# Kernel tuning notes

Measured on AMD Instinct MI355X. Metric: run time of the kernel, lower is better.

## Reference

```python
import jax, jax.numpy as jnp
import numpy as np

H = 1024


def _gru_dir(xg, h0, w_hh, b_hh, reverse):
    # xg: (L, G, 3H) precomputed input-gate projections; h0: (G, H)
    def step(h, xt):
        hg = h @ w_hh.T + b_hh
        xr, xz, xn = jnp.split(xt, 3, axis=-1)
        hr, hz, hn = jnp.split(hg, 3, axis=-1)
        r = jax.nn.sigmoid(xr + hr)
        z = jax.nn.sigmoid(xz + hz)
        n = jnp.tanh(xn + r * hn)
        h_new = (1.0 - z) * n + z * h
        return h_new, h_new
    _, hs = jax.lax.scan(step, h0, xg, reverse=reverse)
    return hs  # (L, G, H), time-ordered (scan reverse keeps original order)


def setup_inputs() -> dict:
    key = jax.random.key(0)
    ks = jax.random.split(key, 12)
    N, G, L = 16384, 256, 128
    s = 1.0 / np.sqrt(H)
    inp = {
        "h_atom": jax.random.normal(ks[0], (N, H), dtype=jnp.float32),
        "batch": jnp.sort(jax.random.randint(ks[1], (N,), 0, G)),
        "bias": jax.random.uniform(ks[2], (H,), jnp.float32, -s, s),
        "w_ih_f": jax.random.uniform(ks[3], (3 * H, H), jnp.float32, -s, s),
        "w_hh_f": jax.random.uniform(ks[4], (3 * H, H), jnp.float32, -s, s),
        "b_ih_f": jax.random.uniform(ks[5], (3 * H,), jnp.float32, -s, s),
        "b_hh_f": jax.random.uniform(ks[6], (3 * H,), jnp.float32, -s, s),
        "w_ih_b": jax.random.uniform(ks[7], (3 * H, H), jnp.float32, -s, s),
        "w_hh_b": jax.random.uniform(ks[8], (3 * H, H), jnp.float32, -s, s),
        "b_ih_b": jax.random.uniform(ks[9], (3 * H,), jnp.float32, -s, s),
        "b_hh_b": jax.random.uniform(ks[10], (3 * H,), jnp.float32, -s, s),
        "num_graphs": G,
        "pad_len": L,
    }
    return inp


def reference(h_atom, bias, w_ih_f, w_hh_f, b_ih_f, b_hh_f,
              w_ih_b, w_hh_b, b_ih_b, b_hh_b, batch, num_graphs, pad_len):
    N = h_atom.shape[0]
    G, L = num_graphs, pad_len
    message = jax.nn.relu(h_atom + bias)  # (N, H)

    # per-graph counts / positions (batch is sorted by graph id)
    counts = jax.ops.segment_sum(jnp.ones((N,), jnp.int32), batch, num_segments=G)
    start = jnp.cumsum(counts) - counts
    pos = jnp.arange(N) - start[batch]  # position of each atom within its graph

    # pad ragged atoms -> (G, L, H); padded slots stay zero (matches torch)
    msgs = jnp.zeros((G, L, H), h_atom.dtype).at[batch, pos].set(message)

    # segment-max hidden init, shared by both directions
    h0 = jax.ops.segment_max(h_atom, batch, num_segments=G)  # (G, H)
    h0 = jnp.where(counts[:, None] > 0, h0, 0.0)

    # precompute input-gate projections, time-major
    xg_f = jnp.einsum('glh,kh->lgk', msgs, w_ih_f) + b_ih_f  # (L, G, 3H)
    xg_b = jnp.einsum('glh,kh->lgk', msgs, w_ih_b) + b_ih_b

    hs_f = _gru_dir(xg_f, h0, w_hh_f, b_hh_f, reverse=False)  # (L, G, H)
    hs_b = _gru_dir(xg_b, h0, w_hh_b, b_hh_b, reverse=True)   # (L, G, H)

    h_messages = jnp.concatenate([hs_f, hs_b], axis=-1).transpose(1, 0, 2)  # (G, L, 2H)

    # unpad back to (N, 2H)
    return h_messages[batch, pos]
```

## Files before the change

### kernel.cpp

```cpp
#include <hip/hip_runtime.h>
#include <stdint.h>

#define H 1024
#define G_ 256
#define LPAD 128

typedef float  floatx4 __attribute__((ext_vector_type(4)));
typedef short  shortx8 __attribute__((ext_vector_type(8)));

#define MFMA(a, b, c) __builtin_amdgcn_mfma_f32_16x16x32_bf16((a), (b), (c), 0, 0, 0)

__device__ __forceinline__ uint16_t f2bf(float f) {
  union { float f; uint32_t i; } v; v.f = f;
  uint32_t r = (v.i + 0x7FFFu + ((v.i >> 16) & 1u)) >> 16;
  return (uint16_t)r;
}
__device__ __forceinline__ float bf2f(uint16_t u) {
  union { uint32_t i; float f; } v; v.i = ((uint32_t)u) << 16; return v.f;
}
__device__ __forceinline__ float sigmoid_(float x) { return 1.f / (1.f + __expf(-x)); }
__device__ __forceinline__ float tanh_(float x) {
  float ax = fabsf(x);
  float e = __expf(2.f * ax);
  float t = 1.f - 2.f / (e + 1.f);
  return x >= 0.f ? t : -t;
}

__global__ void k_f2b(const float* __restrict__ src, uint16_t* __restrict__ dst) {
  size_t i = ((size_t)blockIdx.x * blockDim.x + threadIdx.x) * 8;
  float4 a = *(const float4*)(src + i);
  float4 b = *(const float4*)(src + i + 4);
  uint16_t o[8] = {f2bf(a.x), f2bf(a.y), f2bf(a.z), f2bf(a.w),
                   f2bf(b.x), f2bf(b.y), f2bf(b.z), f2bf(b.w)};
  uint4 ov; __builtin_memcpy(&ov, o, 16);
  *(uint4*)(dst + i) = ov;
}

__global__ void k_setup(const int* __restrict__ batch, int N, int* __restrict__ start,
                        int* __restrict__ bar) {
  int g = threadIdx.x;
  if (g < 512) bar[g] = 0;
  if (g > G_) return;
  int lo = 0, hi = N;
  while (lo < hi) { int mid = (lo + hi) >> 1; if (batch[mid] < g) lo = mid + 1; else hi = mid; }
  start[g] = lo;
}

__global__ void k_msg(const float* __restrict__ h_atom, const float* __restrict__ bias,
                      uint16_t* __restrict__ msg) {
  int row = blockIdx.x, t = threadIdx.x;
  size_t off = (size_t)row * H + t * 8;
  float4 h0 = *(const float4*)(h_atom + off);
  float4 h1 = *(const float4*)(h_atom + off + 4);
  float4 b0 = *(const float4*)(bias + t * 8);
  float4 b1 = *(const float4*)(bias + t * 8 + 4);
  float v[8] = {h0.x + b0.x, h0.y + b0.y, h0.z + b0.z, h0.w + b0.w,
                h1.x + b1.x, h1.y + b1.y, h1.z + b1.z, h1.w + b1.w};
  uint16_t o[8];
#pragma unroll
  for (int i = 0; i < 8; i++) o[i] = f2bf(v[i] > 0.f ? v[i] : 0.f);
  uint4 ov; __builtin_memcpy(&ov, o, 16);
  *(uint4*)(msg + off) = ov;
}

__global__ void k_h0(const float* __restrict__ h_atom, const int* __restrict__ start,
                     float* __restrict__ hf32, uint16_t* __restrict__ hbf) {
  int g = blockIdx.x, t = threadIdx.x;
  int s = start[g], e = start[g + 1];
  float m[4] = {-INFINITY, -INFINITY, -INFINITY, -INFINITY};
  const float* base = h_atom + t * 4;
  for (int a = s; a < e; a++) {
    float4 v = *(const float4*)(base + (size_t)a * H);
    m[0] = fmaxf(m[0], v.x); m[1] = fmaxf(m[1], v.y);
    m[2] = fmaxf(m[2], v.z); m[3] = fmaxf(m[3], v.w);
  }
  if (s == e) { m[0] = m[1] = m[2] = m[3] = 0.f; }
#pragma unroll
  for (int i = 0; i < 4; i++) {
    int c = t * 4 + i;
    float mv = m[i];
    uint16_t bv = f2bf(mv);
    hf32[(size_t)0 * G_ * H + (size_t)g * H + c] = mv;
    hf32[(size_t)2 * G_ * H + (size_t)g * H + c] = mv;
    hbf [(size_t)0 * G_ * H + (size_t)g * H + c] = bv;
    hbf [(size_t)2 * G_ * H + (size_t)g * H + c] = bv;
  }
}

__global__ __launch_bounds__(256) void k_gemm_xg(
    const uint16_t* __restrict__ A, const uint16_t* __restrict__ Wf,
    const uint16_t* __restrict__ Wb, uint16_t* __restrict__ C, int N) {
  __shared__ __align__(16) uint16_t SM[128 * 128];
  uint16_t* As = SM;
  uint16_t* Bs = SM + 128 * 64;
  int bn = blockIdx.x, bm = blockIdx.y;
  const uint16_t* B = (bn < 24) ? Wf : Wb;
  int brow = (bn < 24 ? bn : bn - 24) * 128;
  int tid = threadIdx.x, wid = tid >> 6, lane = tid & 63;
  int wm = wid >> 1, wn = wid & 1;
  floatx4 acc[4][4];
#pragma unroll
  for (int mi = 0; mi < 4; mi++)
#pragma unroll
    for (int ni = 0; ni < 4; ni++) acc[mi][ni] = (floatx4){0.f, 0.f, 0.f, 0.f};
  int arow = bm * 128;
  for (int kb = 0; kb < H; kb += 64) {
    uint4 av[4], bv[4];
#pragma unroll
    for (int p = 0; p < 4; p++) {
      int c = p * 256 + tid;
      av[p] = *(const uint4*)(A + (size_t)(arow + (c >> 3)) * H + kb + (c & 7) * 8);
      bv[p] = *(const uint4*)(B + (size_t)(brow + (c >> 3)) * H + kb + (c & 7) * 8);
    }
    __syncthreads();
#pragma unroll
    for (int p = 0; p < 4; p++) {
      int c = p * 256 + tid;
      *(uint4*)(As + (size_t)c * 8) = av[p];
      *(uint4*)(Bs + (size_t)c * 8) = bv[p];
    }
    __syncthreads();
#pragma unroll
    for (int ks = 0; ks < 2; ks++) {
      const uint16_t* ab = As + ((wm * 64 + (lane & 15)) * 64 + ks * 32 + (lane >> 4) * 8);
      const uint16_t* bb = Bs + ((wn * 64 + (lane & 15)) * 64 + ks * 32 + (lane >> 4) * 8);
      shortx8 af[4], bfr[4];
#pragma unroll
      for (int i = 0; i < 4; i++) {
        af[i]  = *(const shortx8*)(ab + i * 16 * 64);
        bfr[i] = *(const shortx8*)(bb + i * 16 * 64);
      }
#pragma unroll
      for (int mi = 0; mi < 4; mi++)
#pragma unroll
        for (int ni = 0; ni < 4; ni++)
          acc[mi][ni] = MFMA(af[mi], bfr[ni], acc[mi][ni]);
    }
  }
  __syncthreads();
  int crow = wm * 64 + (lane >> 4) * 4;
  int ccol = wn * 64 + (lane & 15);
#pragma unroll
  for (int mi = 0; mi < 4; mi++)
#pragma unroll
    for (int ni = 0; ni < 4; ni++)
#pragma unroll
      for (int r = 0; r < 4; r++)
        SM[(crow + mi * 16 + r) * 128 + ccol + ni * 16] = f2bf(acc[mi][ni][r]);
  __syncthreads();
#pragma unroll
  for (int p = 0; p < 8; p++) {
    int c = p * 256 + tid;
    int row = c >> 4, col = (c & 15) * 8;
    *(uint4*)(C + (size_t)(arow + row) * 6144 + bn * 128 + col) =
        *(const uint4*)(SM + row * 128 + col);
  }
}

__global__ __launch_bounds__(256) void k_gru(
    const uint16_t* __restrict__ xg,
    const uint16_t* __restrict__ whf, const uint16_t* __restrict__ whb,
    const float* __restrict__ bihf, const float* __restrict__ bhhf,
    const float* __restrict__ bihb, const float* __restrict__ bhhb,
    float* __restrict__ hf32, uint16_t* __restrict__ hbf,
    const int* __restrict__ start, float* __restrict__ out,
    int* bar) {
  __shared__ __align__(16) uint16_t As[64 * 64];
  __shared__ __align__(16) uint16_t Bs[96 * 64];
  __shared__ float HG[64 * 97];
  int b = blockIdx.x;
  int e = b & 7, hi = b >> 3;
  int d = e >> 2, jm = e & 3;
  int jc = (hi & 7) * 4 + jm;
  int g0 = (hi >> 3) * 64;
  int grp = d * 4 + (hi >> 3);
  const uint16_t* W = d ? whb : whf;
  int tid = threadIdx.x, wid = tid >> 6, lane = tid & 63;
  int wm = wid >> 1, wn = wid & 1;

  int base = tid * 8;
  int gl = base >> 5, j0 = base & 31;
  int g = g0 + gl;
  int s = start[g], cnt = start[g + 1] - s;
  int col0 = jc * 32 + j0;
  const float* bih = d ? bihb : bihf;
  const float* bhh = d ? bhhb : bhhf;
  float br8[8], bz8[8], bni8[8], bnh8[8];
#pragma unroll
  for (int i = 0; i < 8; i++) {
    int c = col0 + i;
    br8[i] = bih[c] + bhh[c];
    bz8[i] = bih[H + c] + bhh[H + c];
    bni8[i] = bih[2 * H + c];
    bnh8[i] = bhh[2 * H + c];
  }

  int a_row[2], aw_off[2];
#pragma unroll
  for (int p = 0; p < 2; p++) {
    int c = p * 256 + tid, row = c >> 3;
    a_row[p] = row;
    aw_off[p] = row * 128 + (((tid & 7) * 16) ^ ((row & 7) << 4));
  }
  int b_wrow[3], bw_off[3];
#pragma unroll
  for (int p = 0; p < 3; p++) {
    int c = p * 256 + tid, row = c >> 3;
    b_wrow[p] = (row >> 5) * H + jc * 32 + (row & 31);
    bw_off[p] = row * 128 + (((tid & 7) * 16) ^ ((row & 7) << 4));
  }
  int xm = (lane & 7) << 4;
  int arow0 = (wm * 32 + (lane & 15)) * 128;
  int brow0 = (wn * 48 + (lane & 15)) * 128;
  int kchunk = (tid & 7) * 8;

  for (int l = 0; l < LPAD; l++) {
    int cur = l & 1;
    const uint16_t* hsrc = hbf + (size_t)(d * 2 + cur) * G_ * H;
    int t = d ? (LPAD - 1 - l) : l;
    bool active = (t < cnt);

    uint4 xr8 = {0, 0, 0, 0}, xz8 = {0, 0, 0, 0}, xn8 = {0, 0, 0, 0};
    if (active) {
      const uint16_t* xp = xg + (size_t)(s + t) * 6144 + (size_t)d * 3072 + col0;
      xr8 = *(const uint4*)xp;
      xz8 = *(const uint4*)(xp + H);
      xn8 = *(const uint4*)(xp + 2 * H);
    }
    const float* h_old = hf32 + ((size_t)(d * 2 + cur) * G_ + g) * H + col0;
    float4 ho0 = *(const float4*)h_old;
    float4 ho1 = *(const float4*)(h_old + 4);

    floatx4 acc[2][3];
#pragma unroll
    for (int mi = 0; mi < 2; mi++)
#pragma unroll
      for (int ni = 0; ni < 3; ni++) acc[mi][ni] = (floatx4){0.f, 0.f, 0.f, 0.f};

    uint4 av[2], bv[3];
#pragma unroll
    for (int p = 0; p < 2; p++)
      av[p] = *(const uint4*)(hsrc + (size_t)(g0 + a_row[p]) * H + kchunk);
#pragma unroll
    for (int p = 0; p < 3; p++)
      bv[p] = *(const uint4*)(W + (size_t)b_wrow[p] * H + kchunk);

    for (int kb = 0; kb < 16; kb++) {
      __syncthreads();
#pragma unroll
      for (int p = 0; p < 2; p++) *(uint4*)((char*)As + aw_off[p]) = av[p];
#pragma unroll
      for (int p = 0; p < 3; p++) *(uint4*)((char*)Bs + bw_off[p]) = bv[p];
      __syncthreads();
      if (kb < 15) {
        int ko = (kb + 1) * 64 + kchunk;
#pragma unroll
        for (int p = 0; p < 2; p++)
          av[p] = *(const uint4*)(hsrc + (size_t)(g0 + a_row[p]) * H + ko);
#pragma unroll
        for (int p = 0; p < 3; p++)
          bv[p] = *(const uint4*)(W + (size_t)b_wrow[p] * H + ko);
      }
#pragma unroll
      for (int ks = 0; ks < 2; ks++) {
        int o = (ks * 64 + (lane >> 4) * 16) ^ xm;
        shortx8 a0 = *(const shortx8*)((const char*)As + arow0 + o);
        shortx8 a1 = *(const shortx8*)((const char*)As + arow0 + 2048 + o);
#pragma unroll
        for (int ni = 0; ni < 3; ni++) {
          shortx8 bf_ = *(const shortx8*)((const char*)Bs + brow0 + ni * 2048 + o);
          acc[0][ni] = MFMA(a0, bf_, acc[0][ni]);
          acc[1][ni] = MFMA(a1, bf_, acc[1][ni]);
        }
      }
    }
    __syncthreads();
#pragma unroll
    for (int mi = 0; mi < 2; mi++)
#pragma unroll
      for (int ni = 0; ni < 3; ni++) {
        int row0 = wm * 32 + mi * 16 + (lane >> 4) * 4;
        int col = wn * 48 + ni * 16 + (lane & 15);
#pragma unroll
        for (int r = 0; r < 4; r++) HG[(row0 + r) * 97 + col] = acc[mi][ni][r];
      }
    __syncthreads();

    float hv[8] = {ho0.x, ho0.y, ho0.z, ho0.w, ho1.x, ho1.y, ho1.z, ho1.w};
    const uint16_t* xru = (const uint16_t*)&xr8;
    const uint16_t* xzu = (const uint16_t*)&xz8;
    const uint16_t* xnu = (const uint16_t*)&xn8;
    float o32[8]; uint16_t ob[8];
#pragma unroll
    for (int i = 0; i < 8; i++) {
      float hr = HG[gl * 97 + j0 + i];
      float hz = HG[gl * 97 + 32 + j0 + i];
      float hn = HG[gl * 97 + 64 + j0 + i];
      float r = sigmoid_(bf2f(xru[i]) + hr + br8[i]);
      float z = sigmoid_(bf2f(xzu[i]) + hz + bz8[i]);
      float n = tanh_(bf2f(xnu[i]) + bni8[i] + r * (hn + bnh8[i]));
      float hnew = (1.f - z) * n + z * hv[i];
      o32[i] = hnew;
      ob[i] = f2bf(hnew);
    }
    float* h_new32 = hf32 + ((size_t)(d * 2 + (cur ^ 1)) * G_ + g) * H + col0;
    uint16_t* h_newb = hbf + ((size_t)(d * 2 + (cur ^ 1)) * G_ + g) * H + col0;
    *(float4*)h_new32 = make_float4(o32[0], o32[1], o32[2], o32[3]);
    *(float4*)(h_new32 + 4) = make_float4(o32[4], o32[5], o32[6], o32[7]);
    uint4 obv; __builtin_memcpy(&obv, ob, 16);
    *(uint4*)h_newb = obv;
    if (active) {
      float* op = out + (size_t)(s + t) * 2048 + (size_t)d * H + col0;
      *(float4*)op = make_float4(o32[0], o32[1], o32[2], o32[3]);
      *(float4*)(op + 4) = make_float4(o32[4], o32[5], o32[6], o32[7]);
    }

    if (l + 1 < LPAD) {
      __syncthreads();
      if (tid == 0) {
        __threadfence();
        __hip_atomic_fetch_add(&bar[grp * 32], 1, __ATOMIC_RELEASE, __HIP_MEMORY_SCOPE_AGENT);
        int tgt = (l + 1) * 32;
        while (__hip_atomic_load(&bar[grp * 32], __ATOMIC_RELAXED, __HIP_MEMORY_SCOPE_AGENT) < tgt)
          __builtin_amdgcn_s_sleep(2);
        __threadfence();
      }
      __syncthreads();
    }
  }
}

extern "C" void kernel_launch(void* const* d_in, const int* in_sizes, int n_in,
                              void* d_out, int out_size, void* d_ws, size_t ws_size,
                              hipStream_t stream) {
  const float* h_atom = (const float*)d_in[0];
  const int*   batch  = (const int*)d_in[1];
  const float* bias   = (const float*)d_in[2];
  const float* w_ih_f = (const float*)d_in[3];
  const float* w_hh_f = (const float*)d_in[4];
  const float* b_ih_f = (const float*)d_in[5];
  const float* b_hh_f = (const float*)d_in[6];
  const float* w_ih_b = (const float*)d_in[7];
  const float* w_hh_b = (const float*)d_in[8];
  const float* b_ih_b = (const float*)d_in[9];
  const float* b_hh_b = (const float*)d_in[10];
  int N = in_sizes[0] / H;
  float* out = (float*)d_out;

  const size_t W3 = (size_t)3 * H * H;
  char* ws = (char*)d_ws;
  uint16_t* msg  = (uint16_t*)ws;
  uint16_t* xg   = (uint16_t*)(ws + (size_t)N * H * 2);
  char* p = ws + (size_t)N * H * 2 + (size_t)N * 6144 * 2;
  uint16_t* wihf = (uint16_t*)p; p += W3 * 2;
  uint16_t* wihb = (uint16_t*)p; p += W3 * 2;
  uint16_t* whhf = (uint16_t*)p; p += W3 * 2;
  uint16_t* whhb = (uint16_t*)p; p += W3 * 2;
  float*    hf32 = (float*)p;    p += (size_t)4 * G_ * H * 4;
  uint16_t* hbf  = (uint16_t*)p; p += (size_t)4 * G_ * H * 2;
  int*      start = (int*)p;
  int*      bar   = (int*)(p + 2048);

  int wgrid = (int)(W3 / (256 * 8));
  k_f2b<<<wgrid, 256, 0, stream>>>(w_ih_f, wihf);
  k_f2b<<<wgrid, 256, 0, stream>>>(w_ih_b, wihb);
  k_f2b<<<wgrid, 256, 0, stream>>>(w_hh_f, whhf);
  k_f2b<<<wgrid, 256, 0, stream>>>(w_hh_b, whhb);
  k_setup<<<1, 512, 0, stream>>>(batch, N, start, bar);
  k_msg<<<N, 128, 0, stream>>>(h_atom, bias, msg);
  k_h0<<<G_, 256, 0, stream>>>(h_atom, start, hf32, hbf);
  k_gemm_xg<<<dim3(48, N / 128), 256, 0, stream>>>(msg, wihf, wihb, xg, N);

  void* ka[] = {(void*)&xg, (void*)&whhf, (void*)&whhb,
                (void*)&b_ih_f, (void*)&b_hh_f, (void*)&b_ih_b, (void*)&b_hh_b,
                (void*)&hf32, (void*)&hbf, (void*)&start, (void*)&out, (void*)&bar};
  hipLaunchCooperativeKernel(k_gru, dim3(G_), dim3(256), ka, 0, stream);
}
```

Before: 7.435 ms.

## Split GRU recurrent GEMM K across two wave groups and keep fp32 hidden in registers

The recurrent GRU kernel now runs 512 threads per block, with two groups of four waves each handling half of the K=1024 reduction. Their partial results are summed in shared memory before the gate math. The fp32 hidden state is held in per-thread registers across timesteps instead of being read from and written to global memory each step, and the block-to-(direction, graph range, column chunk) mapping is reordered. This is meant to halve the serial K loop per step and remove the global fp32 state traffic, at the cost of larger shared memory, an extra reduction pass, and higher register and occupancy pressure.

```diff
diff --git a/kernel.cpp b/kernel.cpp
--- a/kernel.cpp
+++ b/kernel.cpp
@@ -7,6 +7,7 @@
 
 typedef float  floatx4 __attribute__((ext_vector_type(4)));
 typedef short  shortx8 __attribute__((ext_vector_type(8)));
+typedef uint16_t u16x4 __attribute__((ext_vector_type(4)));
 
 #define MFMA(a, b, c) __builtin_amdgcn_mfma_f32_16x16x32_bf16((a), (b), (c), 0, 0, 0)
 
@@ -157,62 +158,69 @@
   }
 }
 
-__global__ __launch_bounds__(256) void k_gru(
+__global__ __launch_bounds__(512) void k_gru(
     const uint16_t* __restrict__ xg,
     const uint16_t* __restrict__ whf, const uint16_t* __restrict__ whb,
     const float* __restrict__ bihf, const float* __restrict__ bhhf,
     const float* __restrict__ bihb, const float* __restrict__ bhhb,
-    float* __restrict__ hf32, uint16_t* __restrict__ hbf,
+    const float* __restrict__ hf32, uint16_t* __restrict__ hbf,
     const int* __restrict__ start, float* __restrict__ out,
     int* bar) {
-  __shared__ __align__(16) uint16_t As[64 * 64];
-  __shared__ __align__(16) uint16_t Bs[96 * 64];
-  __shared__ float HG[64 * 97];
+  __shared__ __align__(16) char SMEM[49664];
+  char* AsB = SMEM;
+  char* BsB = SMEM + 16384;
+  float* HGf = (float*)SMEM;
+
   int b = blockIdx.x;
-  int e = b & 7, hi = b >> 3;
-  int d = e >> 2, jm = e & 3;
-  int jc = (hi & 7) * 4 + jm;
-  int g0 = (hi >> 3) * 64;
-  int grp = d * 4 + (hi >> 3);
+  int gid = b & 7;
+  int d = gid >> 2, grange = gid & 3;
+  int jc = b >> 3;
+  int g0 = grange * 64;
   const uint16_t* W = d ? whb : whf;
-  int tid = threadIdx.x, wid = tid >> 6, lane = tid & 63;
-  int wm = wid >> 1, wn = wid & 1;
-
-  int base = tid * 8;
-  int gl = base >> 5, j0 = base & 31;
+  int tid = threadIdx.x, lane = tid & 63, wid = tid >> 6;
+  int kh = wid >> 2;
+  int wq = wid & 3, wm = wq >> 1, wn = wq & 1;
+  int th = tid & 255;
+
+  int gl = tid >> 3, j0 = (tid & 7) * 4;
   int g = g0 + gl;
   int s = start[g], cnt = start[g + 1] - s;
   int col0 = jc * 32 + j0;
   const float* bih = d ? bihb : bihf;
   const float* bhh = d ? bhhb : bhhf;
-  float br8[8], bz8[8], bni8[8], bnh8[8];
-#pragma unroll
-  for (int i = 0; i < 8; i++) {
+  float br4[4], bz4[4], bni4[4], bnh4[4];
+#pragma unroll
+  for (int i = 0; i < 4; i++) {
     int c = col0 + i;
-    br8[i] = bih[c] + bhh[c];
-    bz8[i] = bih[H + c] + bhh[H + c];
-    bni8[i] = bih[2 * H + c];
-    bnh8[i] = bhh[2 * H + c];
+    br4[i] = bih[c] + bhh[c];
+    bz4[i] = bih[H + c] + bhh[H + c];
+    bni4[i] = bih[2 * H + c];
+    bnh4[i] = bhh[2 * H + c];
+  }
+  float hreg[4];
+  {
+    float4 h4 = *(const float4*)(hf32 + ((size_t)(d * 2) * G_ + g) * H + col0);
+    hreg[0] = h4.x; hreg[1] = h4.y; hreg[2] = h4.z; hreg[3] = h4.w;
   }
 
   int a_row[2], aw_off[2];
 #pragma unroll
   for (int p = 0; p < 2; p++) {
-    int c = p * 256 + tid, row = c >> 3;
+    int c = p * 256 + th, row = c >> 3;
     a_row[p] = row;
-    aw_off[p] = row * 128 + (((tid & 7) * 16) ^ ((row & 7) << 4));
+    aw_off[p] = kh * 8192 + row * 128 + (((th & 7) * 16) ^ ((row & 7) << 4));
   }
   int b_wrow[3], bw_off[3];
 #pragma unroll
   for (int p = 0; p < 3; p++) {
-    int c = p * 256 + tid, row = c >> 3;
+    int c = p * 256 + th, row = c >> 3;
     b_wrow[p] = (row >> 5) * H + jc * 32 + (row & 31);
-    bw_off[p] = row * 128 + (((tid & 7) * 16) ^ ((row & 7) << 4));
-  }
+    bw_off[p] = kh * 12288 + row * 128 + (((th & 7) * 16) ^ ((row & 7) << 4));
+  }
+  int kchunk = (th & 7) * 8;
   int xm = (lane & 7) << 4;
-  int arow0 = (wm * 32 + (lane & 15)) * 128;
-  int brow0 = (wn * 48 + (lane & 15)) * 128;
-  int kchunk = (tid & 7) * 8;
+  int arow0 = kh * 8192 + (wm * 32 + (lane & 15)) * 128;
+  int brow0 = kh * 12288 + (wn * 48 + (lane & 15)) * 128;
 
   for (int l = 0; l < LPAD; l++) {
     int cur = l & 1;
@@ -220,16 +228,13 @@
     int t = d ? (LPAD - 1 - l) : l;
     bool active = (t < cnt);
 
-    uint4 xr8 = {0, 0, 0, 0}, xz8 = {0, 0, 0, 0}, xn8 = {0, 0, 0, 0};
+    u16x4 xr4 = {0, 0, 0, 0}, xz4 = {0, 0, 0, 0}, xn4 = {0, 0, 0, 0};
     if (active) {
       const uint16_t* xp = xg + (size_t)(s + t) * 6144 + (size_t)d * 3072 + col0;
-      xr8 = *(const uint4*)xp;
-      xz8 = *(const uint4*)(xp + H);
-      xn8 = *(const uint4*)(xp + 2 * H);
-    }
-    const float* h_old = hf32 + ((size_t)(d * 2 + cur) * G_ + g) * H + col0;
-    float4 ho0 = *(const float4*)h_old;
-    float4 ho1 = *(const float4*)(h_old + 4);
+      xr4 = *(const u16x4*)xp;
+      xz4 = *(const u16x4*)(xp + H);
+      xn4 = *(const u16x4*)(xp + 2 * H);
+    }
 
     floatx4 acc[2][3];
 #pragma unroll
@@ -238,22 +243,23 @@
       for (int ni = 0; ni < 3; ni++) acc[mi][ni] = (floatx4){0.f, 0.f, 0.f, 0.f};
 
     uint4 av[2], bv[3];
+    int kbase = kh * 512 + kchunk;
 #pragma unroll
     for (int p = 0; p < 2; p++)
-      av[p] = *(const uint4*)(hsrc + (size_t)(g0 + a_row[p]) * H + kchunk);
+      av[p] = *(const uint4*)(hsrc + (size_t)(g0 + a_row[p]) * H + kbase);
 #pragma unroll
     for (int p = 0; p < 3; p++)
-      bv[p] = *(const uint4*)(W + (size_t)b_wrow[p] * H + kchunk);
-
-    for (int kb = 0; kb < 16; kb++) {
+      bv[p] = *(const uint4*)(W + (size_t)b_wrow[p] * H + kbase);
+
+    for (int kb = 0; kb < 8; kb++) {
       __syncthreads();
 #pragma unroll
-      for (int p = 0; p < 2; p++) *(uint4*)((char*)As + aw_off[p]) = av[p];
-#pragma unroll
-      for (int p = 0; p < 3; p++) *(uint4*)((char*)Bs + bw_off[p]) = bv[p];
+      for (int p = 0; p < 2; p++) *(uint4*)(AsB + aw_off[p]) = av[p];
+#pragma unroll
+      for (int p = 0; p < 3; p++) *(uint4*)(BsB + bw_off[p]) = bv[p];
       __syncthreads();
-      if (kb < 15) {
-        int ko = (kb + 1) * 64 + kchunk;
+      if (kb < 7) {
+        int ko = kh * 512 + (kb + 1) * 64 + kchunk;
 #pragma unroll
         for (int p = 0; p < 2; p++)
           av[p] = *(const uint4*)(hsrc + (size_t)(g0 + a_row[p]) * H + ko);
@@ -264,11 +270,11 @@
 #pragma unroll
       for (int ks = 0; ks < 2; ks++) {
         int o = (ks * 64 + (lane >> 4) * 16) ^ xm;
-        shortx8 a0 = *(const shortx8*)((const char*)As + arow0 + o);
-        shortx8 a1 = *(const shortx8*)((const char*)As + arow0 + 2048 + o);
+        shortx8 a0 = *(const shortx8*)(AsB + arow0 + o);
+        shortx8 a1 = *(const shortx8*)(AsB + arow0 + 2048 + o);
 #pragma unroll
         for (int ni = 0; ni < 3; ni++) {
-          shortx8 bf_ = *(const shortx8*)((const char*)Bs + brow0 + ni * 2048 + o);
+          shortx8 bf_ = *(const shortx8*)(BsB + brow0 + ni * 2048 + o);
           acc[0][ni] = MFMA(a0, bf_, acc[0][ni]);
           acc[1][ni] = MFMA(a1, bf_, acc[1][ni]);
         }
@@ -282,46 +288,44 @@
         int row0 = wm * 32 + mi * 16 + (lane >> 4) * 4;
         int col = wn * 48 + ni * 16 + (lane & 15);
 #pragma unroll
-        for (int r = 0; r < 4; r++) HG[(row0 + r) * 97 + col] = acc[mi][ni][r];
+        for (int r = 0; r < 4; r++)
+          HGf[kh * 6208 + (row0 + r) * 97 + col] = acc[mi][ni][r];
       }
     __syncthreads();
 
-    float hv[8] = {ho0.x, ho0.y, ho0.z, ho0.w, ho1.x, ho1.y, ho1.z, ho1.w};
-    const uint16_t* xru = (const uint16_t*)&xr8;
-    const uint16_t* xzu = (const uint16_t*)&xz8;
-    const uint16_t* xnu = (const uint16_t*)&xn8;
-    float o32[8]; uint16_t ob[8];
-#pragma unroll
-    for (int i = 0; i < 8; i++) {
-      float hr = HG[gl * 97 + j0 + i];
-      float hz = HG[gl * 97 + 32 + j0 + i];
-      float hn = HG[gl * 97 + 64 + j0 + i];
-      float r = sigmoid_(bf2f(xru[i]) + hr + br8[i]);
-      float z = sigmoid_(bf2f(xzu[i]) + hz + bz8[i]);
-      float n = tanh_(bf2f(xnu[i]) + bni8[i] + r * (hn + bnh8[i]));
-      float hnew = (1.f - z) * n + z * hv[i];
-      o32[i] = hnew;
+    const uint16_t* xru = (const uint16_t*)&xr4;
+    const uint16_t* xzu = (const uint16_t*)&xz4;
+    const uint16_t* xnu = (const uint16_t*)&xn4;
+    uint16_t ob[4]; floatx4 ov;
+#pragma unroll
+    for (int i = 0; i < 4; i++) {
+      int hx = gl * 97 + j0 + i;
+      float hr = HGf[hx] + HGf[6208 + hx];
+      float hz = HGf[hx + 32] + HGf[6208 + hx + 32];
+      float hn = HGf[hx + 64] + HGf[6208 + hx + 64];
+      float r = sigmoid_(bf2f(xru[i]) + hr + br4[i]);
+      float z = sigmoid_(bf2f(xzu[i]) + hz + bz4[i]);
+      float n = tanh_(bf2f(xnu[i]) + bni4[i] + r * (hn + bnh4[i]));
+      float hnew = (1.f - z) * n + z * hreg[i];
+      hreg[i] = hnew;
       ob[i] = f2bf(hnew);
-    }
-    float* h_new32 = hf32 + ((size_t)(d * 2 + (cur ^ 1)) * G_ + g) * H + col0;
-    uint16_t* h_newb = hbf + ((size_t)(d * 2 + (cur ^ 1)) * G_ + g) * H + col0;
-    *(float4*)h_new32 = make_float4(o32[0], o32[1], o32[2], o32[3]);
-    *(float4*)(h_new32 + 4) = make_float4(o32[4], o32[5], o32[6], o32[7]);
-    uint4 obv; __builtin_memcpy(&obv, ob, 16);
-    *(uint4*)h_newb = obv;
+      ov[i] = hnew;
+    }
+    uint16_t* hb = hbf + ((size_t)(d * 2 + (cur ^ 1)) * G_ + g) * H + col0;
+    u16x4 obv; __builtin_memcpy(&obv, ob, 8);
+    *(u16x4*)hb = obv;
     if (active) {
       float* op = out + (size_t)(s + t) * 2048 + (size_t)d * H + col0;
-      *(float4*)op = make_float4(o32[0], o32[1], o32[2], o32[3]);
-      *(float4*)(op + 4) = make_float4(o32[4], o32[5], o32[6], o32[7]);
+      *(floatx4*)op = ov;
     }
 
     if (l + 1 < LPAD) {
       __syncthreads();
       if (tid == 0) {
         __threadfence();
-        __hip_atomic_fetch_add(&bar[grp * 32], 1, __ATOMIC_RELEASE, __HIP_MEMORY_SCOPE_AGENT);
+        __hip_atomic_fetch_add(&bar[gid * 32], 1, __ATOMIC_RELEASE, __HIP_MEMORY_SCOPE_AGENT);
         int tgt = (l + 1) * 32;
-        while (__hip_atomic_load(&bar[grp * 32], __ATOMIC_RELAXED, __HIP_MEMORY_SCOPE_AGENT) < tgt)
+        while (__hip_atomic_load(&bar[gid * 32], __ATOMIC_RELAXED, __HIP_MEMORY_SCOPE_AGENT) < tgt)
           __builtin_amdgcn_s_sleep(2);
         __threadfence();
       }
@@ -374,5 +378,5 @@
   void* ka[] = {(void*)&xg, (void*)&whhf, (void*)&whhb,
                 (void*)&b_ih_f, (void*)&b_hh_f, (void*)&b_ih_b, (void*)&b_hh_b,
                 (void*)&hf32, (void*)&hbf, (void*)&start, (void*)&out, (void*)&bar};
-  hipLaunchCooperativeKernel(k_gru, dim3(G_), dim3(256), ka, 0, stream);
-}
+  hipLaunchCooperativeKernel(k_gru, dim3(G_), dim3(512), ka, 0, stream);
+}
```

Measured after the change: 6.697 ms. -9.9%, faster.
